# Kernel tuning notes

Measured on AMD Instinct MI355X. Metric: run time of the kernel, lower is better.

Reference implementation:

```python
import jax, jax.numpy as jnp
import numpy as np

B, T = 1048576, 8
ALPHA = 1.1
COMMISSION = 0.05
BET_PCT = 0.02  # assumed bet_percentage (undefined in original __init__)
TAU = 0.1
EPS = 1e-8


def setup_inputs() -> dict:
    key = jax.random.key(0)
    k1, k2, k3, k4 = jax.random.split(key, 4)
    # network outputs are probabilities (used as probs in entropy/profit terms)
    predicted_probs = jax.nn.softmax(jax.random.normal(k1, (B, T), dtype=jnp.float32), axis=1)
    # one-hot true winners
    winner_idx = jax.random.randint(k2, (B,), 0, T)
    true_winners = jax.nn.one_hot(winner_idx, T, dtype=jnp.float32)
    # decimal odds in [1.5, 15): valid and complete field for nearly all races
    market_odds = jax.random.uniform(k3, (B, T), dtype=jnp.float32, minval=1.5, maxval=15.0)
    # explicit Gumbel(0,1) noise standing in for F.gumbel_softmax's internal sample
    u = jax.random.uniform(k4, (B, T), dtype=jnp.float32, minval=1e-6, maxval=1.0 - 1e-6)
    gumbel_noise = -jnp.log(-jnp.log(u))
    return {"predicted_probs": predicted_probs, "true_winners": true_winners,
            "market_odds": market_odds, "gumbel_noise": gumbel_noise}


def reference(predicted_probs, true_winners, market_odds, gumbel_noise):
    batch_size = predicted_probs.shape[0]
    # race validity
    has_valid_odds = jnp.any(market_odds > 0, axis=1)
    implied_probs = 1.0 / jnp.clip(market_odds, 1.01)
    has_complete_field = implied_probs.sum(axis=1) >= 0.95
    valid = has_valid_odds & has_complete_field  # [B]

    # masked expected profit per dog
    ep = jnp.where(valid[:, None],
                   (market_odds * ALPHA * predicted_probs - 1.0) * BET_PCT * (1.0 - COMMISSION),
                   0.0)  # [B,T]

    # gumbel-softmax selection (logits = ep / temperature, tau = temperature)
    soft_selection = jax.nn.softmax((ep / TAU + gumbel_noise) / TAU, axis=1)
    soft_expected_profits = (soft_selection * ep).sum(axis=1)  # [B]

    # prediction cross-entropy (probs treated as logits, per original code)
    labels = jnp.argmax(true_winners, axis=1)
    logp = jax.nn.log_softmax(predicted_probs, axis=1)
    ce = -jnp.take_along_axis(logp, labels[:, None], axis=1)[:, 0]  # [B]

    valid_f = valid.astype(ce.dtype)
    cnt = valid_f.sum()
    prediction_loss = jnp.where(cnt > 0, (ce * valid_f).sum() / jnp.maximum(cnt, 1.0), ce.mean())

    confidence_penalty = -predicted_probs.max(axis=1).mean() * 0.1
    betting_loss = jnp.where(cnt > 0, -(soft_expected_profits * valid_f).sum() / batch_size,
                             confidence_penalty)

    entropy_reg = -(predicted_probs * jnp.log(predicted_probs + EPS)).sum(axis=1).mean()

    lambda_betting = jnp.minimum(0.5 + cnt / 10000.0 * 0.5, 1.0)
    lambda_entropy = 0.01
    loss = prediction_loss + lambda_betting * betting_loss - lambda_entropy * entropy_reg
    return loss
```

## Files before the change

kernel.cpp:

```cpp
#include <hip/hip_runtime.h>
#include <math.h>


constexpr int T = 8;
constexpr int NB = 2048;
constexpr int NT = 256;
constexpr int RPT = 2;

__device__ __forceinline__ float fastrcp(float x) {
  return __builtin_amdgcn_rcpf(x);
}

__global__ __launch_bounds__(NT, 4) void betting_main(
    const float* __restrict__ pp, const float* __restrict__ tw,
    const float* __restrict__ mo, const float* __restrict__ gn,
    float* __restrict__ partials, int nraces) {
  const int tid = blockIdx.x * NT + threadIdx.x;
  const int ntot = gridDim.x * NT;

  const float4* __restrict__ pp4 = (const float4*)pp;
  const float4* __restrict__ tw4 = (const float4*)tw;
  const float4* __restrict__ mo4 = (const float4*)mo;
  const float4* __restrict__ gn4 = (const float4*)gn;

  float4 A[RPT][2], W[RPT][2], O[RPT][2], G[RPT][2];
  float wgt[RPT];
#pragma unroll
  for (int k = 0; k < RPT; ++k) {
    int r = tid + k * ntot;
    wgt[k] = (r < nraces) ? 1.f : 0.f;
    r = min(r, nraces - 1);
    A[k][0] = pp4[2 * r]; A[k][1] = pp4[2 * r + 1];
    W[k][0] = tw4[2 * r]; W[k][1] = tw4[2 * r + 1];
    O[k][0] = mo4[2 * r]; O[k][1] = mo4[2 * r + 1];
    G[k][0] = gn4[2 * r]; G[k][1] = gn4[2 * r + 1];
  }

  float acc[6] = {0.f, 0.f, 0.f, 0.f, 0.f, 0.f};

#pragma unroll
  for (int k = 0; k < RPT; ++k) {
    float p[T] = {A[k][0].x, A[k][0].y, A[k][0].z, A[k][0].w,
                  A[k][1].x, A[k][1].y, A[k][1].z, A[k][1].w};
    float w[T] = {W[k][0].x, W[k][0].y, W[k][0].z, W[k][0].w,
                  W[k][1].x, W[k][1].y, W[k][1].z, W[k][1].w};
    float o[T] = {O[k][0].x, O[k][0].y, O[k][0].z, O[k][0].w,
                  O[k][1].x, O[k][1].y, O[k][1].z, O[k][1].w};
    float g[T] = {G[k][0].x, G[k][0].y, G[k][0].z, G[k][0].w,
                  G[k][1].x, G[k][1].y, G[k][1].z, G[k][1].w};

    bool anypos = false;
    float simp = 0.f;
#pragma unroll
    for (int t = 0; t < T; ++t) {
      anypos = anypos || (o[t] > 0.f);
      simp += fastrcp(fmaxf(o[t], 1.01f));
    }
    bool valid = anypos && (simp >= 0.95f);
    float vf = valid ? 1.f : 0.f;

    float ep[T];
#pragma unroll
    for (int t = 0; t < T; ++t)
      ep[t] = valid ? (o[t] * 1.1f * p[t] - 1.f) * (0.02f * 0.95f) : 0.f;

    float z[T], zm = -INFINITY;
#pragma unroll
    for (int t = 0; t < T; ++t) {
      z[t] = ep[t] * 100.f + g[t] * 10.f;
      zm = fmaxf(zm, z[t]);
    }
    float s2 = 0.f, sp = 0.f;
#pragma unroll
    for (int t = 0; t < T; ++t) {
      float e = __expf(z[t] - zm);
      s2 += e;
      sp += e * ep[t];
    }
    float soft_ep = sp * fastrcp(s2);

    float m = -INFINITY;
#pragma unroll
    for (int t = 0; t < T; ++t) m = fmaxf(m, p[t]);
    float se = 0.f, plabel = 0.f;
#pragma unroll
    for (int t = 0; t < T; ++t) {
      se += __expf(p[t] - m);
      plabel += w[t] * p[t];
    }
    float ce = m + __logf(se) - plabel;

    float ent = 0.f;
#pragma unroll
    for (int t = 0; t < T; ++t) ent -= p[t] * __logf(p[t] + 1e-8f);

    const float wg = wgt[k];
    acc[0] += vf * wg;
    acc[1] += ce * vf * wg;
    acc[2] += ce * wg;
    acc[3] += soft_ep * vf * wg;
    acc[4] += m * wg;
    acc[5] += ent * wg;
  }

  __shared__ float red[NT / 64][6];
#pragma unroll
  for (int k = 0; k < 6; ++k) {
#pragma unroll
    for (int off = 32; off >= 1; off >>= 1) acc[k] += __shfl_down(acc[k], off);
  }
  int lane = threadIdx.x & 63, wave = threadIdx.x >> 6;
  if (lane == 0) {
#pragma unroll
    for (int k = 0; k < 6; ++k) red[wave][k] = acc[k];
  }
  __syncthreads();
  if (threadIdx.x == 0) {
#pragma unroll
    for (int k = 0; k < 6; ++k) {
      float s = 0.f;
      for (int wv = 0; wv < NT / 64; ++wv) s += red[wv][k];
      partials[k * gridDim.x + blockIdx.x] = s;
    }
  }
}

__global__ __launch_bounds__(NT) void betting_final(
    const float* __restrict__ partials, int nb, float* __restrict__ out,
    double Bd) {
  __shared__ double red[NT / 64][6];
  double a[6] = {0, 0, 0, 0, 0, 0};
#pragma unroll
  for (int k = 0; k < 6; ++k)
    for (int i = threadIdx.x; i < nb; i += NT) a[k] += (double)partials[k * nb + i];
#pragma unroll
  for (int k = 0; k < 6; ++k) {
#pragma unroll
    for (int off = 32; off >= 1; off >>= 1) a[k] += __shfl_down(a[k], off);
  }
  int lane = threadIdx.x & 63, wave = threadIdx.x >> 6;
  if (lane == 0) {
#pragma unroll
    for (int k = 0; k < 6; ++k) red[wave][k] = a[k];
  }
  __syncthreads();
  if (threadIdx.x == 0) {
    double s[6];
#pragma unroll
    for (int k = 0; k < 6; ++k) {
      s[k] = 0.0;
      for (int wv = 0; wv < NT / 64; ++wv) s[k] += red[wv][k];
    }
    double cnt = s[0], Scev = s[1], Sce = s[2], Ssoft = s[3], Smax = s[4],
           Sent = s[5];
    double pred = (cnt > 0.0) ? Scev / fmax(cnt, 1.0) : Sce / Bd;
    double conf = -(Smax / Bd) * 0.1;
    double bet = (cnt > 0.0) ? -Ssoft / Bd : conf;
    double ent = Sent / Bd;
    double lam = fmin(0.5 + cnt / 10000.0 * 0.5, 1.0);
    out[0] = (float)(pred + lam * bet - 0.01 * ent);
  }
}

extern "C" void kernel_launch(void* const* d_in, const int* in_sizes, int n_in,
                              void* d_out, int out_size, void* d_ws,
                              size_t ws_size, hipStream_t stream) {
  const float* pp = (const float*)d_in[0];
  const float* tw = (const float*)d_in[1];
  const float* mo = (const float*)d_in[2];
  const float* gn = (const float*)d_in[3];
  float* out = (float*)d_out;
  float* partials = (float*)d_ws;

  int nraces = in_sizes[0] / T;

  betting_main<<<NB, NT, 0, stream>>>(pp, tw, mo, gn, partials, nraces);
  betting_final<<<1, NT, 0, stream>>>(partials, NB, out, (double)nraces);
}
```

Baseline: 40.75 us.

## Fuse final reduction via last-block atomic and software-pipeline race loads

Merges the separate final-reduction kernel into the main kernel: each block writes its partials and increments an atomic counter, and the last block to finish does the double-precision final sum. The main loop now processes four races per thread, prefetching the next race's loads while computing the current one, with a grid sized exactly to the problem (1024 blocks). It also drops the per-element validity select in ep by folding validity into the weights. This adds a memset launch for the counter and relies on the acq_rel atomic for cross-block visibility.

```diff
diff --git a/kernel.cpp b/kernel.cpp
--- a/kernel.cpp
+++ b/kernel.cpp
@@ -2,178 +2,219 @@
 #include <math.h>
 
 
-constexpr int T = 8;
-constexpr int NB = 2048;
 constexpr int NT = 256;
-constexpr int RPT = 2;
 
 __device__ __forceinline__ float fastrcp(float x) {
   return __builtin_amdgcn_rcpf(x);
 }
 
-__global__ __launch_bounds__(NT, 4) void betting_main(
-    const float* __restrict__ pp, const float* __restrict__ tw,
-    const float* __restrict__ mo, const float* __restrict__ gn,
-    float* __restrict__ partials, int nraces) {
-  const int tid = blockIdx.x * NT + threadIdx.x;
-  const int ntot = gridDim.x * NT;
-
-  const float4* __restrict__ pp4 = (const float4*)pp;
-  const float4* __restrict__ tw4 = (const float4*)tw;
-  const float4* __restrict__ mo4 = (const float4*)mo;
-  const float4* __restrict__ gn4 = (const float4*)gn;
-
-  float4 A[RPT][2], W[RPT][2], O[RPT][2], G[RPT][2];
-  float wgt[RPT];
-#pragma unroll
-  for (int k = 0; k < RPT; ++k) {
-    int r = tid + k * ntot;
-    wgt[k] = (r < nraces) ? 1.f : 0.f;
-    r = min(r, nraces - 1);
-    A[k][0] = pp4[2 * r]; A[k][1] = pp4[2 * r + 1];
-    W[k][0] = tw4[2 * r]; W[k][1] = tw4[2 * r + 1];
-    O[k][0] = mo4[2 * r]; O[k][1] = mo4[2 * r + 1];
-    G[k][0] = gn4[2 * r]; G[k][1] = gn4[2 * r + 1];
-  }
-
-  float acc[6] = {0.f, 0.f, 0.f, 0.f, 0.f, 0.f};
-
-#pragma unroll
-  for (int k = 0; k < RPT; ++k) {
-    float p[T] = {A[k][0].x, A[k][0].y, A[k][0].z, A[k][0].w,
-                  A[k][1].x, A[k][1].y, A[k][1].z, A[k][1].w};
-    float w[T] = {W[k][0].x, W[k][0].y, W[k][0].z, W[k][0].w,
-                  W[k][1].x, W[k][1].y, W[k][1].z, W[k][1].w};
-    float o[T] = {O[k][0].x, O[k][0].y, O[k][0].z, O[k][0].w,
-                  O[k][1].x, O[k][1].y, O[k][1].z, O[k][1].w};
-    float g[T] = {G[k][0].x, G[k][0].y, G[k][0].z, G[k][0].w,
-                  G[k][1].x, G[k][1].y, G[k][1].z, G[k][1].w};
-
-    bool anypos = false;
-    float simp = 0.f;
-#pragma unroll
-    for (int t = 0; t < T; ++t) {
-      anypos = anypos || (o[t] > 0.f);
-      simp += fastrcp(fmaxf(o[t], 1.01f));
+struct Race {
+  float4 a0, a1, w0, w1, o0, o1, g0, g1;
+};
+
+__device__ __forceinline__ void load_race(const float4* __restrict__ pp,
+                                          const float4* __restrict__ tw,
+                                          const float4* __restrict__ mo,
+                                          const float4* __restrict__ gn,
+                                          int r, Race& R) {
+  R.a0 = pp[2 * r]; R.a1 = pp[2 * r + 1];
+  R.w0 = tw[2 * r]; R.w1 = tw[2 * r + 1];
+  R.o0 = mo[2 * r]; R.o1 = mo[2 * r + 1];
+  R.g0 = gn[2 * r]; R.g1 = gn[2 * r + 1];
+}
+
+__device__ __forceinline__ void compute_race(const Race& R, float wg,
+                                             float acc[6]) {
+  float p[8] = {R.a0.x, R.a0.y, R.a0.z, R.a0.w, R.a1.x, R.a1.y, R.a1.z, R.a1.w};
+  float w[8] = {R.w0.x, R.w0.y, R.w0.z, R.w0.w, R.w1.x, R.w1.y, R.w1.z, R.w1.w};
+  float o[8] = {R.o0.x, R.o0.y, R.o0.z, R.o0.w, R.o1.x, R.o1.y, R.o1.z, R.o1.w};
+  float g[8] = {R.g0.x, R.g0.y, R.g0.z, R.g0.w, R.g1.x, R.g1.y, R.g1.z, R.g1.w};
+
+  bool anypos = false;
+  float simp = 0.f;
+#pragma unroll
+  for (int t = 0; t < 8; ++t) {
+    anypos = anypos || (o[t] > 0.f);
+    simp += fastrcp(fmaxf(o[t], 1.01f));
+  }
+  float vfw = (anypos && simp >= 0.95f) ? wg : 0.f;
+
+  float ep[8];
+#pragma unroll
+  for (int t = 0; t < 8; ++t)
+    ep[t] = (o[t] * 1.1f * p[t] - 1.f) * (0.02f * 0.95f);
+
+  float z[8], zm = -INFINITY;
+#pragma unroll
+  for (int t = 0; t < 8; ++t) {
+    z[t] = ep[t] * 100.f + g[t] * 10.f;
+    zm = fmaxf(zm, z[t]);
+  }
+  float s2 = 0.f, sp = 0.f;
+#pragma unroll
+  for (int t = 0; t < 8; ++t) {
+    float e = __expf(z[t] - zm);
+    s2 += e;
+    sp += e * ep[t];
+  }
+  float soft_ep = sp * fastrcp(s2);
+
+  float m = -INFINITY;
+#pragma unroll
+  for (int t = 0; t < 8; ++t) m = fmaxf(m, p[t]);
+  float se = 0.f, pl = 0.f;
+#pragma unroll
+  for (int t = 0; t < 8; ++t) {
+    se += __expf(p[t] - m);
+    pl += w[t] * p[t];
+  }
+  float ce = m + __logf(se) - pl;
+
+  float ent = 0.f;
+#pragma unroll
+  for (int t = 0; t < 8; ++t) ent -= p[t] * __logf(p[t] + 1e-8f);
+
+  acc[0] += vfw;
+  acc[1] += ce * vfw;
+  acc[2] += ce * wg;
+  acc[3] += soft_ep * vfw;
+  acc[4] += m * wg;
+  acc[5] += ent * wg;
+}
+
+__device__ __forceinline__ void reduce_and_finish(float acc[6],
+                                                  float* __restrict__ partials,
+                                                  unsigned* __restrict__ counter,
+                                                  float* __restrict__ out,
+                                                  int nb, double Bd) {
+  __shared__ float red[NT / 64][6];
+#pragma unroll
+  for (int k = 0; k < 6; ++k) {
+#pragma unroll
+    for (int off = 32; off >= 1; off >>= 1) acc[k] += __shfl_down(acc[k], off);
+  }
+  const int lane = threadIdx.x & 63, wave = threadIdx.x >> 6;
+  if (lane == 0) {
+#pragma unroll
+    for (int k = 0; k < 6; ++k) red[wave][k] = acc[k];
+  }
+  __syncthreads();
+
+  __shared__ int slast;
+  if (threadIdx.x == 0) {
+#pragma unroll
+    for (int k = 0; k < 6; ++k) {
+      float s = red[0][k] + red[1][k] + red[2][k] + red[3][k];
+      partials[k * nb + blockIdx.x] = s;
     }
-    bool valid = anypos && (simp >= 0.95f);
-    float vf = valid ? 1.f : 0.f;
-
-    float ep[T];
-#pragma unroll
-    for (int t = 0; t < T; ++t)
-      ep[t] = valid ? (o[t] * 1.1f * p[t] - 1.f) * (0.02f * 0.95f) : 0.f;
-
-    float z[T], zm = -INFINITY;
-#pragma unroll
-    for (int t = 0; t < T; ++t) {
-      z[t] = ep[t] * 100.f + g[t] * 10.f;
-      zm = fmaxf(zm, z[t]);
-    }
-    float s2 = 0.f, sp = 0.f;
-#pragma unroll
-    for (int t = 0; t < T; ++t) {
-      float e = __expf(z[t] - zm);
-      s2 += e;
-      sp += e * ep[t];
-    }
-    float soft_ep = sp * fastrcp(s2);
-
-    float m = -INFINITY;
-#pragma unroll
-    for (int t = 0; t < T; ++t) m = fmaxf(m, p[t]);
-    float se = 0.f, plabel = 0.f;
-#pragma unroll
-    for (int t = 0; t < T; ++t) {
-      se += __expf(p[t] - m);
-      plabel += w[t] * p[t];
-    }
-    float ce = m + __logf(se) - plabel;
-
-    float ent = 0.f;
-#pragma unroll
-    for (int t = 0; t < T; ++t) ent -= p[t] * __logf(p[t] + 1e-8f);
-
-    const float wg = wgt[k];
-    acc[0] += vf * wg;
-    acc[1] += ce * vf * wg;
-    acc[2] += ce * wg;
-    acc[3] += soft_ep * vf * wg;
-    acc[4] += m * wg;
-    acc[5] += ent * wg;
-  }
-
-  __shared__ float red[NT / 64][6];
+    unsigned c = __hip_atomic_fetch_add(counter, 1u, __ATOMIC_ACQ_REL,
+                                        __HIP_MEMORY_SCOPE_AGENT);
+    slast = (c == (unsigned)(nb - 1));
+  }
+  __syncthreads();
+  if (!slast) return;
+
+  __shared__ double redd[NT / 64][6];
+  double a[6] = {0, 0, 0, 0, 0, 0};
+#pragma unroll
+  for (int k = 0; k < 6; ++k)
+    for (int i = threadIdx.x; i < nb; i += NT)
+      a[k] += (double)__hip_atomic_load(&partials[k * nb + i], __ATOMIC_RELAXED,
+                                        __HIP_MEMORY_SCOPE_AGENT);
 #pragma unroll
   for (int k = 0; k < 6; ++k) {
 #pragma unroll
-    for (int off = 32; off >= 1; off >>= 1) acc[k] += __shfl_down(acc[k], off);
-  }
-  int lane = threadIdx.x & 63, wave = threadIdx.x >> 6;
+    for (int off = 32; off >= 1; off >>= 1) a[k] += __shfl_down(a[k], off);
+  }
   if (lane == 0) {
 #pragma unroll
-    for (int k = 0; k < 6; ++k) red[wave][k] = acc[k];
-  }
-  __syncthreads();
-  if (threadIdx.x == 0) {
-#pragma unroll
-    for (int k = 0; k < 6; ++k) {
-      float s = 0.f;
-      for (int wv = 0; wv < NT / 64; ++wv) s += red[wv][k];
-      partials[k * gridDim.x + blockIdx.x] = s;
-    }
-  }
-}
-
-__global__ __launch_bounds__(NT) void betting_final(
-    const float* __restrict__ partials, int nb, float* __restrict__ out,
-    double Bd) {
-  __shared__ double red[NT / 64][6];
-  double a[6] = {0, 0, 0, 0, 0, 0};
-#pragma unroll
-  for (int k = 0; k < 6; ++k)
-    for (int i = threadIdx.x; i < nb; i += NT) a[k] += (double)partials[k * nb + i];
-#pragma unroll
-  for (int k = 0; k < 6; ++k) {
-#pragma unroll
-    for (int off = 32; off >= 1; off >>= 1) a[k] += __shfl_down(a[k], off);
-  }
-  int lane = threadIdx.x & 63, wave = threadIdx.x >> 6;
-  if (lane == 0) {
-#pragma unroll
-    for (int k = 0; k < 6; ++k) red[wave][k] = a[k];
+    for (int k = 0; k < 6; ++k) redd[wave][k] = a[k];
   }
   __syncthreads();
   if (threadIdx.x == 0) {
     double s[6];
 #pragma unroll
-    for (int k = 0; k < 6; ++k) {
-      s[k] = 0.0;
-      for (int wv = 0; wv < NT / 64; ++wv) s[k] += red[wv][k];
-    }
+    for (int k = 0; k < 6; ++k)
+      s[k] = redd[0][k] + redd[1][k] + redd[2][k] + redd[3][k];
     double cnt = s[0], Scev = s[1], Sce = s[2], Ssoft = s[3], Smax = s[4],
            Sent = s[5];
     double pred = (cnt > 0.0) ? Scev / fmax(cnt, 1.0) : Sce / Bd;
     double conf = -(Smax / Bd) * 0.1;
     double bet = (cnt > 0.0) ? -Ssoft / Bd : conf;
-    double ent = Sent / Bd;
+    double entr = Sent / Bd;
     double lam = fmin(0.5 + cnt / 10000.0 * 0.5, 1.0);
-    out[0] = (float)(pred + lam * bet - 0.01 * ent);
-  }
+    out[0] = (float)(pred + lam * bet - 0.01 * entr);
+  }
+}
+
+template <int NITER>
+__global__ __launch_bounds__(NT, 2) void betting_pipe(
+    const float4* __restrict__ pp, const float4* __restrict__ tw,
+    const float4* __restrict__ mo, const float4* __restrict__ gn,
+    float* __restrict__ partials, unsigned* __restrict__ counter,
+    float* __restrict__ out, int nraces) {
+  const int tid0 = blockIdx.x * NT + threadIdx.x;
+  const int ntot = gridDim.x * NT;
+
+  float acc[6] = {0.f, 0.f, 0.f, 0.f, 0.f, 0.f};
+  Race cur, nxt;
+  load_race(pp, tw, mo, gn, tid0, cur);
+#pragma unroll
+  for (int it = 0; it < NITER; ++it) {
+    if (it + 1 < NITER) load_race(pp, tw, mo, gn, tid0 + (it + 1) * ntot, nxt);
+    compute_race(cur, 1.0f, acc);
+    if (it + 1 < NITER) cur = nxt;
+  }
+
+  reduce_and_finish(acc, partials, counter, out, gridDim.x, (double)nraces);
+}
+
+__global__ __launch_bounds__(NT, 2) void betting_generic(
+    const float4* __restrict__ pp, const float4* __restrict__ tw,
+    const float4* __restrict__ mo, const float4* __restrict__ gn,
+    float* __restrict__ partials, unsigned* __restrict__ counter,
+    float* __restrict__ out, int nraces) {
+  const int tid0 = blockIdx.x * NT + threadIdx.x;
+  const int ntot = gridDim.x * NT;
+
+  float acc[6] = {0.f, 0.f, 0.f, 0.f, 0.f, 0.f};
+  for (int r = tid0; r < nraces; r += ntot) {
+    Race R;
+    load_race(pp, tw, mo, gn, r, R);
+    compute_race(R, 1.0f, acc);
+  }
+  reduce_and_finish(acc, partials, counter, out, gridDim.x, (double)nraces);
 }
 
 extern "C" void kernel_launch(void* const* d_in, const int* in_sizes, int n_in,
                               void* d_out, int out_size, void* d_ws,
                               size_t ws_size, hipStream_t stream) {
-  const float* pp = (const float*)d_in[0];
-  const float* tw = (const float*)d_in[1];
-  const float* mo = (const float*)d_in[2];
-  const float* gn = (const float*)d_in[3];
+  const float4* pp = (const float4*)d_in[0];
+  const float4* tw = (const float4*)d_in[1];
+  const float4* mo = (const float4*)d_in[2];
+  const float4* gn = (const float4*)d_in[3];
   float* out = (float*)d_out;
+
+  const int nraces = in_sizes[0] / 8;
+  constexpr int NITER = 4;
+
+  bool exact = (nraces % (NT * NITER) == 0) && nraces > 0;
+  int grid = exact ? nraces / (NT * NITER) : 1024;
+  while ((size_t)((6 * grid + 1) * 4) > ws_size && grid > 64) {
+    grid >>= 1;
+    exact = false;
+  }
+  if (exact && grid != nraces / (NT * NITER)) exact = false;
+
   float* partials = (float*)d_ws;
-
-  int nraces = in_sizes[0] / T;
-
-  betting_main<<<NB, NT, 0, stream>>>(pp, tw, mo, gn, partials, nraces);
-  betting_final<<<1, NT, 0, stream>>>(partials, NB, out, (double)nraces);
-}
+  unsigned* counter = (unsigned*)(partials + 6 * grid);
+  hipMemsetAsync(counter, 0, sizeof(unsigned), stream);
+
+  if (exact) {
+    betting_pipe<NITER><<<grid, NT, 0, stream>>>(pp, tw, mo, gn, partials,
+                                                 counter, out, nraces);
+  } else {
+    betting_generic<<<grid, NT, 0, stream>>>(pp, tw, mo, gn, partials, counter,
+                                             out, nraces);
+  }
+}
```

Result: slower. 67.48 us (+65.6%).
